# Kernel tuning notes

Measured on AMD Instinct MI355X. Metric: run time of the kernel, lower is better.

## Reference

```python
import jax, jax.numpy as jnp
import numpy as np

N_NODES = 50000


def setup_inputs() -> dict:
    key = jax.random.key(0)
    k1, k2, k3, k4 = jax.random.split(key, 4)
    N, E, F_IN, F_OUT = N_NODES, 1600000, 512, 128
    x = jax.random.normal(k1, (N, F_IN), dtype=jnp.float32)
    edge_index = jax.random.randint(k2, (2, E), 0, N, dtype=jnp.int64)
    edge_weight = jax.random.uniform(k3, (E,), dtype=jnp.float32)
    # glorot init for weight, zeros bias (as in the original layer)
    limit = np.sqrt(6.0 / (F_IN + F_OUT)).astype(np.float32)
    weight = jax.random.uniform(k4, (F_IN, F_OUT), dtype=jnp.float32,
                                minval=-limit, maxval=limit)
    bias = jnp.zeros((F_OUT,), dtype=jnp.float32)
    return {"x": x, "edge_index": edge_index, "edge_weight": edge_weight,
            "weight": weight, "bias": bias}


def reference(x, edge_index, edge_weight, weight, bias):
    # dropout rate is 0 in this config -> identity
    h = x @ weight                                # [N, F_out] dense transform
    src, dst = edge_index[0], edge_index[1]
    # support @ h : sparse adjacency aggregation (SpMM) via gather + segment_sum
    msgs = h[src] * edge_weight[:, None]          # [E, F_out]
    agg = jax.ops.segment_sum(msgs, dst, num_segments=N_NODES)  # [N, F_out]
    return jax.nn.relu(agg + bias)
```

## Files before the change

kernel.cpp:

```cpp
#include <hip/hip_runtime.h>

#define F_IN  512
#define F_OUT 128
#define FBIN  32
#define EPB   4096
#define C2MAX 1600
#define CAPF  2048

typedef __attribute__((ext_vector_type(8))) short  short8;
typedef __attribute__((ext_vector_type(4))) float  floatx4;

__device__ __forceinline__ unsigned short f2bf(float f) {
    unsigned u = __float_as_uint(f);
    return (unsigned short)((u + 0x7FFF + ((u >> 16) & 1)) >> 16);
}
__device__ __forceinline__ float bf2f(unsigned b) {
    return __uint_as_float(b << 16);
}

__global__ __launch_bounds__(256) void prep(
    const float* __restrict__ w, unsigned short* __restrict__ wt,
    int* __restrict__ cursor, int C2)
{
    const int tid = threadIdx.x;
    if ((int)blockIdx.x < 128) {
        int g0 = blockIdx.x * 512 + tid;
        #pragma unroll
        for (int r = 0; r < 2; ++r) {
            int gid = g0 + r * 256;
            int n = gid >> 9, k = gid & 511;
            wt[gid] = f2bf(w[(size_t)k * F_OUT + n]);
        }
    } else {
        int c = ((int)blockIdx.x - 128) * 256 + tid;
        if (c < C2) cursor[c] = 0;
    }
}

__global__ __launch_bounds__(256, 2) void fill_gemm(
    const int* __restrict__ ei, const float* __restrict__ ew,
    int* __restrict__ cursor, uint2* __restrict__ ent, int E, int C2, int FB,
    const float* __restrict__ x, const unsigned short* __restrict__ wt,
    unsigned short* __restrict__ h, int N)
{
    __shared__ __align__(16) char smem[(64 * 68 + 128 * 68) * 2];
    const int tid = threadIdx.x;

    if ((int)blockIdx.x < FB) {
        int* lh    = (int*)smem;
        int* lbase = (int*)smem + C2MAX;
        for (int c = tid; c < C2; c += 256) lh[c] = 0;
        __syncthreads();

        const int base = blockIdx.x * EPB;
        unsigned       mykey[EPB / 256];
        unsigned char  mydl[EPB / 256];
        short          mybin[EPB / 256];
        unsigned short myrank[EPB / 256];

        #pragma unroll
        for (int j = 0; j < EPB / 256; ++j) {
            int e = base + j * 256 + tid;
            mybin[j] = -1;
            if (e < E) {
                int   src = ei[e];
                int   dst = ei[E + e];
                float w   = ew[e];
                int bin = dst >> 5;
                mykey[j]  = (unsigned)src | ((unsigned)f2bf(w) << 16);
                mydl[j]   = (unsigned char)(dst & (FBIN - 1));
                mybin[j]  = (short)bin;
                myrank[j] = (unsigned short)atomicAdd(&lh[bin], 1);
            }
        }
        __syncthreads();
        for (int c = tid; c < C2; c += 256)
            if (lh[c] > 0) lbase[c] = atomicAdd(&cursor[c], lh[c]);
        __syncthreads();
        #pragma unroll
        for (int j = 0; j < EPB / 256; ++j) {
            if (mybin[j] >= 0) {
                int o = lbase[mybin[j]] + myrank[j];
                if (o < CAPF)
                    ent[(size_t)(int)mybin[j] * CAPF + o] = make_uint2(mykey[j], mydl[j]);
            }
        }
        return;
    }

    unsigned short* sa = (unsigned short*)smem;
    unsigned short* sb = sa + 64 * 68;

    const int wave = tid >> 6, lane = tid & 63;
    const int g    = lane >> 4, l16 = lane & 15;
    const int m0   = ((int)blockIdx.x - FB) * 64;

    const int arow = tid >> 2, aq = tid & 3;
    const int brow = tid >> 1, bh = tid & 1;

    floatx4 acc[8];
    #pragma unroll
    for (int i = 0; i < 8; ++i) acc[i] = (floatx4)(0.f);

    const bool  avalid = (m0 + arow) < N;
    const float* xp = x + (size_t)(m0 + arow) * F_IN + aq * 16;
    const unsigned short* bp = wt + brow * F_IN + bh * 32;

    float4 ax[4];
    uint4  bv[4];
    #pragma unroll
    for (int i = 0; i < 4; ++i) ax[i] = make_float4(0.f, 0.f, 0.f, 0.f);
    if (avalid) {
        #pragma unroll
        for (int i = 0; i < 4; ++i) ax[i] = ((const float4*)xp)[i];
    }
    #pragma unroll
    for (int i = 0; i < 4; ++i) bv[i] = ((const uint4*)bp)[i];

    for (int s = 0; s < 8; ++s) {
        __syncthreads();
        #pragma unroll
        for (int i = 0; i < 4; ++i) {
            ushort4 t;
            t.x = f2bf(ax[i].x); t.y = f2bf(ax[i].y);
            t.z = f2bf(ax[i].z); t.w = f2bf(ax[i].w);
            *(ushort4*)&sa[arow * 68 + aq * 16 + i * 4] = t;
        }
        #pragma unroll
        for (int i = 0; i < 4; ++i) {
            *(uint2*)&sb[brow * 68 + bh * 32 + i * 8]     = make_uint2(bv[i].x, bv[i].y);
            *(uint2*)&sb[brow * 68 + bh * 32 + i * 8 + 4] = make_uint2(bv[i].z, bv[i].w);
        }
        if (s < 7) {
            int k0n = (s + 1) * 64;
            if (avalid) {
                #pragma unroll
                for (int i = 0; i < 4; ++i) ax[i] = ((const float4*)(xp + k0n))[i];
            }
            #pragma unroll
            for (int i = 0; i < 4; ++i) bv[i] = ((const uint4*)(bp + k0n))[i];
        }
        __syncthreads();

        #pragma unroll
        for (int kc = 0; kc < 2; ++kc) {
            union { ushort4 u[2]; short8 v; } af;
            int abase = (wave * 16 + l16) * 68 + kc * 32 + g * 8;
            af.u[0] = *(ushort4*)&sa[abase];
            af.u[1] = *(ushort4*)&sa[abase + 4];
            #pragma unroll
            for (int nt = 0; nt < 8; ++nt) {
                union { ushort4 u[2]; short8 v; } bf;
                int bbase = (nt * 16 + l16) * 68 + kc * 32 + g * 8;
                bf.u[0] = *(ushort4*)&sb[bbase];
                bf.u[1] = *(ushort4*)&sb[bbase + 4];
                acc[nt] = __builtin_amdgcn_mfma_f32_16x16x32_bf16(af.v, bf.v, acc[nt], 0, 0, 0);
            }
        }
    }

    #pragma unroll
    for (int nt = 0; nt < 8; ++nt) {
        #pragma unroll
        for (int r = 0; r < 4; ++r) {
            int row = m0 + wave * 16 + g * 4 + r;
            if (row < N) h[(size_t)row * F_OUT + nt * 16 + l16] = f2bf(acc[nt][r]);
        }
    }
}

__global__ __launch_bounds__(256) void fine_agg(
    const unsigned short* __restrict__ h, const uint2* __restrict__ ent,
    const int* __restrict__ cursor, const float* __restrict__ bias,
    float* __restrict__ out, int N, int E,
    const int* __restrict__ ei, const float* __restrict__ ew)
{
    __shared__ unsigned ssort[CAPF];
    __shared__ int lh[FBIN], lcur[FBIN];
    __shared__ int sso[FBIN + 1];

    const int b    = blockIdx.x;
    const int tid  = threadIdx.x;
    const int wave = tid >> 6;
    const int lane = tid & 63;
    const int half = lane >> 5;
    const int q    = lane & 31;
    const float4 bv = *(const float4*)&bias[q * 4];
    const int raw  = cursor[b];
    const int cnt  = raw < CAPF ? raw : CAPF;
    const uint2* slab = ent + (size_t)b * CAPF;

    if (tid < FBIN) lh[tid] = 0;
    __syncthreads();

    for (int i = tid; i < cnt; i += 256)
        atomicAdd(&lh[(int)slab[i].y], 1);
    __syncthreads();

    if (wave == 0 && lane < FBIN) {
        int v = lh[lane];
        int orig = v;
        #pragma unroll
        for (int off = 1; off < FBIN; off <<= 1) {
            int t = __shfl_up(v, off);
            if (lane >= off) v += t;
        }
        sso[lane]  = v - orig;
        lcur[lane] = v - orig;
        if (lane == FBIN - 1) sso[FBIN] = v;
    }
    __syncthreads();

    if (raw <= CAPF) {
        for (int i = tid; i < cnt; i += 256) {
            uint2 e = slab[i];
            int r = atomicAdd(&lcur[(int)e.y], 1);
            ssort[r] = e.x;
        }
        __syncthreads();

        #pragma unroll 1
        for (int t = 0; t < 8; ++t) {
            int nd   = wave * 8 + t;
            int node = b * FBIN + nd;
            int s = sso[nd], e2 = sso[nd + 1];
            float4 acc = make_float4(0.f, 0.f, 0.f, 0.f);
            for (int i = s; i < e2; i += 8) {
                #pragma unroll
                for (int j = 0; j < 4; ++j) {
                    int idx = i + j * 2 + half;
                    unsigned bk = 0;
                    if (idx < e2) bk = ssort[idx];
                    float wgt = bf2f(bk >> 16);
                    uint2 hv = *(const uint2*)&h[(size_t)(bk & 0xFFFF) * F_OUT + q * 4];
                    acc.x += bf2f(hv.x & 0xFFFF) * wgt;
                    acc.y += bf2f(hv.x >> 16)    * wgt;
                    acc.z += bf2f(hv.y & 0xFFFF) * wgt;
                    acc.w += bf2f(hv.y >> 16)    * wgt;
                }
            }
            acc.x += __shfl_xor(acc.x, 32);
            acc.y += __shfl_xor(acc.y, 32);
            acc.z += __shfl_xor(acc.z, 32);
            acc.w += __shfl_xor(acc.w, 32);
            if (half == 0 && node < N) {
                float4 o;
                o.x = fmaxf(acc.x + bv.x, 0.f);
                o.y = fmaxf(acc.y + bv.y, 0.f);
                o.z = fmaxf(acc.z + bv.z, 0.f);
                o.w = fmaxf(acc.w + bv.w, 0.f);
                *(float4*)&out[(size_t)node * F_OUT + q * 4] = o;
            }
        }
    } else {
        #pragma unroll 1
        for (int t = 0; t < 8; ++t) {
            int nd   = wave * 8 + t;
            int node = b * FBIN + nd;
            float4 acc = make_float4(0.f, 0.f, 0.f, 0.f);
            for (int e = half; e < E; e += 2) {
                if (ei[E + e] == node) {
                    float wgt = ew[e];
                    uint2 hv = *(const uint2*)&h[(size_t)ei[e] * F_OUT + q * 4];
                    acc.x += bf2f(hv.x & 0xFFFF) * wgt;
                    acc.y += bf2f(hv.x >> 16)    * wgt;
                    acc.z += bf2f(hv.y & 0xFFFF) * wgt;
                    acc.w += bf2f(hv.y >> 16)    * wgt;
                }
            }
            acc.x += __shfl_xor(acc.x, 32);
            acc.y += __shfl_xor(acc.y, 32);
            acc.z += __shfl_xor(acc.z, 32);
            acc.w += __shfl_xor(acc.w, 32);
            if (half == 0 && node < N) {
                float4 o;
                o.x = fmaxf(acc.x + bv.x, 0.f);
                o.y = fmaxf(acc.y + bv.y, 0.f);
                o.z = fmaxf(acc.z + bv.z, 0.f);
                o.w = fmaxf(acc.w + bv.w, 0.f);
                *(float4*)&out[(size_t)node * F_OUT + q * 4] = o;
            }
        }
    }
}

static inline size_t align256(size_t x) { return (x + 255) & ~(size_t)255; }

extern "C" void kernel_launch(void* const* d_in, const int* in_sizes, int n_in,
                              void* d_out, int out_size, void* d_ws, size_t ws_size,
                              hipStream_t stream)
{
    const float* x    = (const float*)d_in[0];
    const int*   ei   = (const int*)  d_in[1];
    const float* ew   = (const float*)d_in[2];
    const float* w    = (const float*)d_in[3];
    const float* bias = (const float*)d_in[4];
    float*       out  = (float*)d_out;

    const int N  = in_sizes[0] / F_IN;
    const int E  = in_sizes[2];
    const int C2 = (N + FBIN - 1) / FBIN;

    char*  ws = (char*)d_ws;
    size_t off = 0;
    unsigned short* h      = (unsigned short*)(ws + off); off += align256((size_t)N * F_OUT * 2);
    unsigned short* wt     = (unsigned short*)(ws + off); off += align256((size_t)F_OUT * F_IN * 2);
    int*            cursor = (int*)(ws + off);            off += align256((size_t)C2 * 4);
    uint2*          ent    = (uint2*)(ws + off);          off += align256((size_t)C2 * CAPF * 8);

    const int FB = (E + EPB - 1) / EPB;
    const int GB = (N + 63) / 64;
    const int ZB = (C2 + 255) / 256;

    prep<<<128 + ZB, 256, 0, stream>>>(w, wt, cursor, C2);
    fill_gemm<<<FB + GB, 256, 0, stream>>>(ei, ew, cursor, ent, E, C2, FB,
                                           x, wt, h, N);
    fine_agg<<<C2, 256, 0, stream>>>(h, ent, cursor, bias, out, N, E, ei, ew);
}
```

Measured before the change: 252.2 us.

## Use 32x32 MFMA tiles in GEMM and two-pass bucketing with larger fill blocks

The GEMM path switches from 16x16x32 MFMA to 32x32x16 MFMA with a 2x2 wave tiling, so each wave computes a 32x64 output tile. This reduces LDS fragment loads per MFMA. The bucketing fill now handles 16384 edges per block in two passes: a histogram pass, then a second pass that re-reads the edges and scatters them. This drops the per-thread register arrays, but each edge's dst is read twice and there are fewer fill blocks to overlap with the GEMM blocks.

```diff
diff --git a/kernel.cpp b/kernel.cpp
--- a/kernel.cpp
+++ b/kernel.cpp
@@ -3,12 +3,13 @@
 #define F_IN  512
 #define F_OUT 128
 #define FBIN  32
-#define EPB   4096
+#define EPB   16384
 #define C2MAX 1600
 #define CAPF  2048
 
-typedef __attribute__((ext_vector_type(8))) short  short8;
-typedef __attribute__((ext_vector_type(4))) float  floatx4;
+typedef __attribute__((ext_vector_type(8)))  short  short8;
+typedef __attribute__((ext_vector_type(4)))  float  floatx4;
+typedef __attribute__((ext_vector_type(16))) float  floatx16;
 
 __device__ __forceinline__ unsigned short f2bf(float f) {
     unsigned u = __float_as_uint(f);
@@ -53,36 +54,35 @@
         __syncthreads();
 
         const int base = blockIdx.x * EPB;
-        unsigned       mykey[EPB / 256];
-        unsigned char  mydl[EPB / 256];
-        short          mybin[EPB / 256];
-        unsigned short myrank[EPB / 256];
-
-        #pragma unroll
+
+        #pragma unroll 4
         for (int j = 0; j < EPB / 256; ++j) {
             int e = base + j * 256 + tid;
-            mybin[j] = -1;
+            if (e < E) atomicAdd(&lh[ei[E + e] >> 5], 1);
+        }
+        __syncthreads();
+
+        for (int c = tid; c < C2; c += 256) {
+            int v = lh[c];
+            if (v > 0) lbase[c] = atomicAdd(&cursor[c], v);
+            lh[c] = 0;
+        }
+        __syncthreads();
+
+        #pragma unroll 4
+        for (int j = 0; j < EPB / 256; ++j) {
+            int e = base + j * 256 + tid;
             if (e < E) {
                 int   src = ei[e];
                 int   dst = ei[E + e];
                 float w   = ew[e];
                 int bin = dst >> 5;
-                mykey[j]  = (unsigned)src | ((unsigned)f2bf(w) << 16);
-                mydl[j]   = (unsigned char)(dst & (FBIN - 1));
-                mybin[j]  = (short)bin;
-                myrank[j] = (unsigned short)atomicAdd(&lh[bin], 1);
-            }
-        }
-        __syncthreads();
-        for (int c = tid; c < C2; c += 256)
-            if (lh[c] > 0) lbase[c] = atomicAdd(&cursor[c], lh[c]);
-        __syncthreads();
-        #pragma unroll
-        for (int j = 0; j < EPB / 256; ++j) {
-            if (mybin[j] >= 0) {
-                int o = lbase[mybin[j]] + myrank[j];
+                unsigned key = (unsigned)src | ((unsigned)f2bf(w) << 16);
+                int r = atomicAdd(&lh[bin], 1);
+                int o = lbase[bin] + r;
                 if (o < CAPF)
-                    ent[(size_t)(int)mybin[j] * CAPF + o] = make_uint2(mykey[j], mydl[j]);
+                    ent[(size_t)bin * CAPF + o] =
+                        make_uint2(key, (unsigned)(dst & (FBIN - 1)));
             }
         }
         return;
@@ -92,15 +92,16 @@
     unsigned short* sb = sa + 64 * 68;
 
     const int wave = tid >> 6, lane = tid & 63;
-    const int g    = lane >> 4, l16 = lane & 15;
+    const int wm   = wave >> 1, wn = wave & 1;
+    const int lr   = lane & 31, hi = lane >> 5;
     const int m0   = ((int)blockIdx.x - FB) * 64;
 
     const int arow = tid >> 2, aq = tid & 3;
     const int brow = tid >> 1, bh = tid & 1;
 
-    floatx4 acc[8];
+    floatx16 acc[2];
     #pragma unroll
-    for (int i = 0; i < 8; ++i) acc[i] = (floatx4)(0.f);
+    for (int i = 0; i < 2; ++i) acc[i] = (floatx16)(0.f);
 
     const bool  avalid = (m0 + arow) < N;
     const float* xp = x + (size_t)(m0 + arow) * F_IN + aq * 16;
@@ -143,28 +144,29 @@
         __syncthreads();
 
         #pragma unroll
-        for (int kc = 0; kc < 2; ++kc) {
+        for (int kc = 0; kc < 4; ++kc) {
             union { ushort4 u[2]; short8 v; } af;
-            int abase = (wave * 16 + l16) * 68 + kc * 32 + g * 8;
+            int abase = (wm * 32 + lr) * 68 + kc * 16 + hi * 8;
             af.u[0] = *(ushort4*)&sa[abase];
             af.u[1] = *(ushort4*)&sa[abase + 4];
             #pragma unroll
-            for (int nt = 0; nt < 8; ++nt) {
+            for (int nt = 0; nt < 2; ++nt) {
                 union { ushort4 u[2]; short8 v; } bf;
-                int bbase = (nt * 16 + l16) * 68 + kc * 32 + g * 8;
+                int bbase = (wn * 64 + nt * 32 + lr) * 68 + kc * 16 + hi * 8;
                 bf.u[0] = *(ushort4*)&sb[bbase];
                 bf.u[1] = *(ushort4*)&sb[bbase + 4];
-                acc[nt] = __builtin_amdgcn_mfma_f32_16x16x32_bf16(af.v, bf.v, acc[nt], 0, 0, 0);
+                acc[nt] = __builtin_amdgcn_mfma_f32_32x32x16_bf16(af.v, bf.v, acc[nt], 0, 0, 0);
             }
         }
     }
 
     #pragma unroll
-    for (int nt = 0; nt < 8; ++nt) {
-        #pragma unroll
-        for (int r = 0; r < 4; ++r) {
-            int row = m0 + wave * 16 + g * 4 + r;
-            if (row < N) h[(size_t)row * F_OUT + nt * 16 + l16] = f2bf(acc[nt][r]);
+    for (int nt = 0; nt < 2; ++nt) {
+        #pragma unroll
+        for (int r = 0; r < 16; ++r) {
+            int row = m0 + wm * 32 + (r & 3) + 8 * (r >> 2) + 4 * hi;
+            int col = wn * 64 + nt * 32 + lr;
+            if (row < N) h[(size_t)row * F_OUT + col] = f2bf(acc[nt][r]);
         }
     }
 }
```

Measured after the change: 313.4 us. +24.3%, slower.
